# Optimization experiments

Hardware: AMD Instinct MI355X
Metric: run time of the kernel (lower is better)

Reference implementation:

```python
import jax, jax.numpy as jnp
import numpy as np

B, T, C, H, Wimg = 16, 6, 4, 420, 312
PH, PW = 14, 12
E = 768
GH, GW = H // PH, Wimg // PW  # 30, 26 -> 780 patches
N_VALID = 390


def setup_inputs() -> dict:
    key = jax.random.key(0)
    kx, kw, kb = jax.random.split(key, 3)
    x = jax.random.normal(kx, (B, T, C, H, Wimg), dtype=jnp.float32)
    W = jax.random.normal(kw, (E, C, PH, PW), dtype=jnp.float32) * 0.02
    b = jax.random.normal(kb, (E,), dtype=jnp.float32) * 0.02
    # static patch mask: keep half the patches (unique, sorted indices like torch.nonzero)
    rng = np.random.default_rng(0)
    valid = np.sort(rng.choice(GH * GW, size=N_VALID, replace=False)).astype(np.int32)
    return {"x": x, "W": W, "b": b, "valid_indices": jnp.asarray(valid)}


def reference(x, W, b, valid_indices):
    Bv, Tv, Cv, Hv, Wv = x.shape
    Ev, _, ph, pw = W.shape
    gh, gw = Hv // ph, Wv // pw
    # non-overlapping stride=kernel conv == patchify + GEMM
    xp = x.reshape(Bv * Tv, Cv, gh, ph, gw, pw)
    out = jnp.einsum('ncipjq,ecpq->nije', xp, W) + b  # [B*T, gh, gw, E]
    out = out.reshape(Bv, Tv, gh * gw, Ev)            # [B, T, n_patches, E]
    return out[:, :, valid_indices, :]                # [B, T, n_valid, E]
```

## Files before the change

### kernel.cpp

```cpp
#include <hip/hip_runtime.h>

#define M_TOT 37440
#define N_E   768
#define K_TOT 672
#define NV    390
#define GWID  26
#define PHh   14
#define PWw   12
#define IMW   312
#define CSTRIDE 131040
#define NSTRIDE 524160

typedef short bf16x8 __attribute__((ext_vector_type(8)));
typedef float f32x4  __attribute__((ext_vector_type(4)));
typedef unsigned short u16;
typedef u16 u16x4 __attribute__((ext_vector_type(4)));
typedef u16 u16x8 __attribute__((ext_vector_type(8)));

#define ROWB 104

static __device__ __forceinline__ u16 f2bf(float f) {
  unsigned u = __builtin_bit_cast(unsigned, f);
  u = (u + 0x7FFFu + ((u >> 16) & 1u)) >> 16;
  return (u16)u;
}

__global__ __launch_bounds__(256) void patch_gemm(
    const float* __restrict__ x, const float* __restrict__ w,
    const float* __restrict__ bias, const int* __restrict__ valid,
    float* __restrict__ out) {
  __shared__ u16 Alds[128 * ROWB];
  __shared__ u16 Blds[128 * ROWB];

  const int tid  = threadIdx.x;
  const int lane = tid & 63;
  const int wid  = tid >> 6;
  const int wr   = wid >> 1, wc = wid & 1;
  const int lrow = lane & 15, lhi = lane >> 4;

  const int m0 = blockIdx.x * 128;
  const int n0 = blockIdx.y * 128;

  const int arow = tid & 127;
  int m = m0 + arow;
  if (m >= M_TOT) m = M_TOT - 1;
  const int nimg = m / NV;
  const int v    = m - nimg * NV;
  const int g    = valid[v];
  const int gi   = g / GWID;
  const int gj   = g - gi * GWID;
  const float* xrow = x + (size_t)nimg * NSTRIDE + (size_t)(gi * PHh) * IMW + gj * PWw;

  const int half = tid >> 7;
  const float* wrow = w + (size_t)(n0 + arow) * K_TOT;

  f32x4 acc[4][4];
  #pragma unroll
  for (int i = 0; i < 4; ++i)
    #pragma unroll
    for (int j = 0; j < 4; ++j)
      acc[i][j] = (f32x4){0.f, 0.f, 0.f, 0.f};

  for (int t = 0; t < 7; ++t) {
    #pragma unroll
    for (int it = 0; it < 4; ++it) {
      const int run = half + it * 2;
      const int rr  = t * 8 + run;
      const int c   = rr / PHh;
      const int p   = rr - c * PHh;
      const float* src = xrow + (size_t)c * CSTRIDE + p * IMW;
      f32x4 f0 = *(const f32x4*)(src + 0);
      f32x4 f1 = *(const f32x4*)(src + 4);
      f32x4 f2 = *(const f32x4*)(src + 8);
      u16x4 h0 = {f2bf(f0.x), f2bf(f0.y), f2bf(f0.z), f2bf(f0.w)};
      u16x4 h1 = {f2bf(f1.x), f2bf(f1.y), f2bf(f1.z), f2bf(f1.w)};
      u16x4 h2 = {f2bf(f2.x), f2bf(f2.y), f2bf(f2.z), f2bf(f2.w)};
      u16* dst = &Alds[arow * ROWB + run * 12];
      *(u16x4*)(dst + 0) = h0;
      *(u16x4*)(dst + 4) = h1;
      *(u16x4*)(dst + 8) = h2;
    }
    #pragma unroll
    for (int i = 0; i < 6; ++i) {
      const int col = half * 48 + i * 8;
      const float* src = wrow + t * 96 + col;
      f32x4 f0 = *(const f32x4*)(src + 0);
      f32x4 f1 = *(const f32x4*)(src + 4);
      u16x8 h = {f2bf(f0.x), f2bf(f0.y), f2bf(f0.z), f2bf(f0.w),
                 f2bf(f1.x), f2bf(f1.y), f2bf(f1.z), f2bf(f1.w)};
      *(u16x8*)&Blds[arow * ROWB + col] = h;
    }
    __syncthreads();
    #pragma unroll
    for (int kk = 0; kk < 3; ++kk) {
      bf16x8 a[4], b[4];
      #pragma unroll
      for (int i = 0; i < 4; ++i)
        a[i] = *(const bf16x8*)&Alds[(wr * 64 + i * 16 + lrow) * ROWB + kk * 32 + lhi * 8];
      #pragma unroll
      for (int j = 0; j < 4; ++j)
        b[j] = *(const bf16x8*)&Blds[(wc * 64 + j * 16 + lrow) * ROWB + kk * 32 + lhi * 8];
      #pragma unroll
      for (int i = 0; i < 4; ++i)
        #pragma unroll
        for (int j = 0; j < 4; ++j)
          acc[i][j] = __builtin_amdgcn_mfma_f32_16x16x32_bf16(a[i], b[j], acc[i][j], 0, 0, 0);
    }
    __syncthreads();
  }

  float bv[4];
  #pragma unroll
  for (int j = 0; j < 4; ++j)
    bv[j] = bias[n0 + wc * 64 + j * 16 + lrow];

  #pragma unroll
  for (int i = 0; i < 4; ++i) {
    const int mbase = m0 + wr * 64 + i * 16 + lhi * 4;
    #pragma unroll
    for (int j = 0; j < 4; ++j) {
      const int e = n0 + wc * 64 + j * 16 + lrow;
      float* op = out + (size_t)mbase * N_E + e;
      #pragma unroll
      for (int tt = 0; tt < 4; ++tt) {
        if (mbase + tt < M_TOT) op[(size_t)tt * N_E] = acc[i][j][tt] + bv[j];
      }
    }
  }
}

extern "C" void kernel_launch(void* const* d_in, const int* in_sizes, int n_in,
                              void* d_out, int out_size, void* d_ws, size_t ws_size,
                              hipStream_t stream) {
  const float* x     = (const float*)d_in[0];
  const float* w     = (const float*)d_in[1];
  const float* b     = (const float*)d_in[2];
  const int*   valid = (const int*)d_in[3];
  float* out = (float*)d_out;
  dim3 grid((M_TOT + 127) / 128, N_E / 128);
  patch_gemm<<<grid, dim3(256), 0, stream>>>(x, w, b, valid, out);
}
```

Baseline: 450.6 us.

## Split into bf16 patchify pre-pass and direct-to-LDS GEMM kernel

Adds a pre-pass kernel that gathers valid patches and converts x and W to bf16 in a contiguous workspace. A separate GEMM kernel then streams tiles with global_load_lds straight into LDS, with N as the fast grid dimension so blocks sharing an A tile run together. The goal is to stop the six N-tile blocks from each re-reading and re-converting the fp32 gather of x, and to remove register staging. In exchange it adds an extra launch and about 50 MB of workspace write plus read, and falls back to the fused kernel when the workspace is too small.

New measurement: 377.2 us. 16.3% less time.

```diff
diff --git a/kernel.cpp b/kernel.cpp
--- a/kernel.cpp
+++ b/kernel.cpp
@@ -17,7 +17,12 @@
 typedef u16 u16x4 __attribute__((ext_vector_type(4)));
 typedef u16 u16x8 __attribute__((ext_vector_type(8)));
 
-#define ROWB 104
+#define A_WS_BYTES 50319360u
+#define W_WS_ELEMS 516096
+#define WS_NEEDED (A_WS_BYTES + W_WS_ELEMS*2)
+
+#define NBLK_A 8190
+#define NBLK_W 252
 
 static __device__ __forceinline__ u16 f2bf(float f) {
   unsigned u = __builtin_bit_cast(unsigned, f);
@@ -25,22 +30,143 @@
   return (u16)u;
 }
 
-__global__ __launch_bounds__(256) void patch_gemm(
+#define GLOAD_LDS16(g, l) \
+  __builtin_amdgcn_global_load_lds((const __attribute__((address_space(1))) void*)(g), \
+                                   (__attribute__((address_space(3))) void*)(l), 16, 0, 0)
+
+__global__ __launch_bounds__(256) void patchify(
+    const float* __restrict__ x, const float* __restrict__ w,
+    const int* __restrict__ valid, u16* __restrict__ A, u16* __restrict__ Wb) {
+  const int bid = blockIdx.x;
+  const int tid = threadIdx.x;
+  if (bid < NBLK_A) {
+    const int g  = bid * 256 + tid;
+    const int m  = g / 56;
+    const int rr = g - m * 56;
+    const int nimg = m / NV;
+    const int v    = m - nimg * NV;
+    const int gidx = valid[v];
+    const int gi = gidx / GWID, gj = gidx - gi * GWID;
+    const int c  = rr / PHh,    p  = rr - c * PHh;
+    const float* src = x + (size_t)nimg * NSTRIDE + (size_t)c * CSTRIDE
+                         + (size_t)(gi * PHh + p) * IMW + gj * PWw;
+    f32x4 f0 = *(const f32x4*)(src + 0);
+    f32x4 f1 = *(const f32x4*)(src + 4);
+    f32x4 f2 = *(const f32x4*)(src + 8);
+    u16* dst = A + (size_t)m * K_TOT + rr * 12;
+    u16x8 h01 = {f2bf(f0.x), f2bf(f0.y), f2bf(f0.z), f2bf(f0.w),
+                 f2bf(f1.x), f2bf(f1.y), f2bf(f1.z), f2bf(f1.w)};
+    u16x4 h2  = {f2bf(f2.x), f2bf(f2.y), f2bf(f2.z), f2bf(f2.w)};
+    *(u16x8*)(dst + 0) = h01;
+    *(u16x4*)(dst + 8) = h2;
+  } else {
+    const int g = (bid - NBLK_A) * 256 + tid;
+    const float* src = w + (size_t)g * 8;
+    f32x4 f0 = *(const f32x4*)(src + 0);
+    f32x4 f1 = *(const f32x4*)(src + 4);
+    u16x8 h = {f2bf(f0.x), f2bf(f0.y), f2bf(f0.z), f2bf(f0.w),
+               f2bf(f1.x), f2bf(f1.y), f2bf(f1.z), f2bf(f1.w)};
+    *(u16x8*)(Wb + (size_t)g * 8) = h;
+  }
+}
+
+__global__ __launch_bounds__(256) void gemm_bf16(
+    const u16* __restrict__ A, const u16* __restrict__ Bw,
+    const float* __restrict__ bias, float* __restrict__ out) {
+  __shared__ u16 Alds[128 * 96];
+  __shared__ u16 Blds[128 * 96];
+  char* AldsB = (char*)Alds;
+  char* BldsB = (char*)Blds;
+
+  const int tid  = threadIdx.x;
+  const int lane = tid & 63;
+  const int wid  = tid >> 6;
+  const int wr   = wid >> 1, wc = wid & 1;
+  const int lrow = lane & 15, lhi = lane >> 4;
+
+  const int n0 = blockIdx.x * 128;
+  const int m0 = blockIdx.y * 128;
+
+  int aoff[6], boff[6];
+  #pragma unroll
+  for (int j = 0; j < 6; ++j) {
+    const int ci  = wid * 384 + j * 64 + lane;
+    const int row = ci / 12;
+    const int c16 = ci - row * 12;
+    int ar = m0 + row; if (ar >= M_TOT) ar = M_TOT - 1;
+    aoff[j] = ar * K_TOT + c16 * 8;
+    boff[j] = (n0 + row) * K_TOT + c16 * 8;
+  }
+
+  f32x4 acc[4][4];
+  #pragma unroll
+  for (int i = 0; i < 4; ++i)
+    #pragma unroll
+    for (int j = 0; j < 4; ++j)
+      acc[i][j] = (f32x4){0.f, 0.f, 0.f, 0.f};
+
+  for (int t = 0; t < 7; ++t) {
+    const int kb = t * 96;
+    #pragma unroll
+    for (int j = 0; j < 6; ++j)
+      GLOAD_LDS16(A + aoff[j] + kb, AldsB + (wid * 6 + j) * 1024);
+    #pragma unroll
+    for (int j = 0; j < 6; ++j)
+      GLOAD_LDS16(Bw + boff[j] + kb, BldsB + (wid * 6 + j) * 1024);
+    __syncthreads();
+
+    #pragma unroll
+    for (int kk = 0; kk < 3; ++kk) {
+      bf16x8 a[4], b[4];
+      #pragma unroll
+      for (int i = 0; i < 4; ++i)
+        a[i] = *(const bf16x8*)&Alds[(wr * 64 + i * 16 + lrow) * 96 + kk * 32 + lhi * 8];
+      #pragma unroll
+      for (int j = 0; j < 4; ++j)
+        b[j] = *(const bf16x8*)&Blds[(wc * 64 + j * 16 + lrow) * 96 + kk * 32 + lhi * 8];
+      #pragma unroll
+      for (int i = 0; i < 4; ++i)
+        #pragma unroll
+        for (int j = 0; j < 4; ++j)
+          acc[i][j] = __builtin_amdgcn_mfma_f32_16x16x32_bf16(a[i], b[j], acc[i][j], 0, 0, 0);
+    }
+    __syncthreads();
+  }
+
+  float bv[4];
+  #pragma unroll
+  for (int j = 0; j < 4; ++j)
+    bv[j] = bias[n0 + wc * 64 + j * 16 + lrow];
+
+  #pragma unroll
+  for (int i = 0; i < 4; ++i) {
+    const int mbase = m0 + wr * 64 + i * 16 + lhi * 4;
+    #pragma unroll
+    for (int j = 0; j < 4; ++j) {
+      const int e = n0 + wc * 64 + j * 16 + lrow;
+      float* op = out + (size_t)mbase * N_E + e;
+      #pragma unroll
+      for (int tt = 0; tt < 4; ++tt) {
+        if (mbase + tt < M_TOT) op[(size_t)tt * N_E] = acc[i][j][tt] + bv[j];
+      }
+    }
+  }
+}
+
+#define ROWB 104
+__global__ __launch_bounds__(256) void patch_gemm_fused(
     const float* __restrict__ x, const float* __restrict__ w,
     const float* __restrict__ bias, const int* __restrict__ valid,
     float* __restrict__ out) {
   __shared__ u16 Alds[128 * ROWB];
   __shared__ u16 Blds[128 * ROWB];
-
   const int tid  = threadIdx.x;
   const int lane = tid & 63;
   const int wid  = tid >> 6;
   const int wr   = wid >> 1, wc = wid & 1;
   const int lrow = lane & 15, lhi = lane >> 4;
-
   const int m0 = blockIdx.x * 128;
   const int n0 = blockIdx.y * 128;
-
   const int arow = tid & 127;
   int m = m0 + arow;
   if (m >= M_TOT) m = M_TOT - 1;
@@ -50,17 +176,14 @@
   const int gi   = g / GWID;
   const int gj   = g - gi * GWID;
   const float* xrow = x + (size_t)nimg * NSTRIDE + (size_t)(gi * PHh) * IMW + gj * PWw;
-
   const int half = tid >> 7;
   const float* wrow = w + (size_t)(n0 + arow) * K_TOT;
-
   f32x4 acc[4][4];
   #pragma unroll
   for (int i = 0; i < 4; ++i)
     #pragma unroll
     for (int j = 0; j < 4; ++j)
       acc[i][j] = (f32x4){0.f, 0.f, 0.f, 0.f};
-
   for (int t = 0; t < 7; ++t) {
     #pragma unroll
     for (int it = 0; it < 4; ++it) {
@@ -108,12 +231,10 @@
     }
     __syncthreads();
   }
-
   float bv[4];
   #pragma unroll
   for (int j = 0; j < 4; ++j)
     bv[j] = bias[n0 + wc * 64 + j * 16 + lrow];
-
   #pragma unroll
   for (int i = 0; i < 4; ++i) {
     const int mbase = m0 + wr * 64 + i * 16 + lhi * 4;
@@ -137,6 +258,15 @@
   const float* b     = (const float*)d_in[2];
   const int*   valid = (const int*)d_in[3];
   float* out = (float*)d_out;
-  dim3 grid((M_TOT + 127) / 128, N_E / 128);
-  patch_gemm<<<grid, dim3(256), 0, stream>>>(x, w, b, valid, out);
-}
+
+  if (ws_size >= (size_t)WS_NEEDED) {
+    u16* Aws = (u16*)d_ws;
+    u16* Wws = (u16*)((char*)d_ws + A_WS_BYTES);
+    patchify<<<NBLK_A + NBLK_W, 256, 0, stream>>>(x, w, valid, Aws, Wws);
+    dim3 grid(N_E / 128, (M_TOT + 127) / 128);
+    gemm_bf16<<<grid, dim3(256), 0, stream>>>(Aws, Wws, b, out);
+  } else {
+    dim3 grid((M_TOT + 127) / 128, N_E / 128);
+    patch_gemm_fused<<<grid, dim3(256), 0, stream>>>(x, w, b, valid, out);
+  }
+}
```
